# Kernel tuning notes

Measured on AMD Instinct MI355X. Metric: run time of the kernel, lower is better.

Reference implementation:

```python
import jax, jax.numpy as jnp
import numpy as np

N_HEADS = 16
HEAD_DIM = 64


def apply_rope(x, cos, sin):
    # x: [B, H, S, D]; cos/sin: [S, D//2]
    x_even = x[..., ::2]
    x_odd = x[..., 1::2]
    c = cos[None, None, :, :]
    s = sin[None, None, :, :]
    rot_even = x_even * c - x_odd * s
    rot_odd = x_even * s + x_odd * c
    return jnp.stack((rot_even, rot_odd), axis=-1).reshape(x.shape)


def setup_inputs() -> dict:
    key = jax.random.key(0)
    ks = jax.random.split(key, 7)
    B, S, D = 2, 2048, 1024
    x = jax.random.normal(ks[0], (B, S, D), dtype=jnp.float32)
    # realistic rope tables
    inv_freq = 1.0 / (10000.0 ** (np.arange(0, HEAD_DIM, 2, dtype=np.float32) / HEAD_DIM))
    t = np.arange(S, dtype=np.float32)
    freqs = np.outer(t, inv_freq)  # [S, HEAD_DIM//2]
    rope_cos = jnp.asarray(np.cos(freqs), dtype=jnp.float32)
    rope_sin = jnp.asarray(np.sin(freqs), dtype=jnp.float32)
    Wqkv = jax.random.normal(ks[1], (D, 3 * D), dtype=jnp.float32) * (D ** -0.5)
    bqkv = jax.random.normal(ks[2], (3 * D,), dtype=jnp.float32) * 0.02
    Wout = jax.random.normal(ks[3], (D, D), dtype=jnp.float32) * (D ** -0.5)
    bout = jax.random.normal(ks[4], (D,), dtype=jnp.float32) * 0.02
    return {"x": x, "rope_cos": rope_cos, "rope_sin": rope_sin,
            "Wqkv": Wqkv, "bqkv": bqkv, "Wout": Wout, "bout": bout}


def reference(x, rope_cos, rope_sin, Wqkv, bqkv, Wout, bout):
    B, S, D = x.shape
    H, Hd = N_HEADS, HEAD_DIM
    qkv = x @ Wqkv + bqkv                      # [B, S, 3D]
    qkv = qkv.reshape(B, S, 3, H, Hd).transpose(2, 0, 3, 1, 4)  # [3, B, H, S, Hd]
    q, k, v = qkv[0], qkv[1], qkv[2]
    q = apply_rope(q, rope_cos, rope_sin)
    k = apply_rope(k, rope_cos, rope_sin)
    scale = Hd ** -0.5
    scores = jnp.einsum('bhqd,bhkd->bhqk', q, k) * scale
    causal = jnp.tril(jnp.ones((S, S), dtype=bool))
    scores = jnp.where(causal[None, None], scores, jnp.finfo(scores.dtype).min)
    attn = jax.nn.softmax(scores, axis=-1)
    out = jnp.einsum('bhqk,bhkd->bhqd', attn, v)  # [B, H, S, Hd]
    out = out.transpose(0, 2, 1, 3).reshape(B, S, D)
    return out @ Wout + bout
```

## Files before the change

### kernel.cpp

```cpp
#include <hip/hip_runtime.h>
#include <hip/hip_bf16.h>

typedef unsigned short u16;
typedef __attribute__((ext_vector_type(4))) float f32x4;
typedef __attribute__((ext_vector_type(16))) float f32x16;
typedef __attribute__((ext_vector_type(8))) short short8;
typedef __attribute__((ext_vector_type(8))) unsigned short ushort8;

__device__ __forceinline__ u16 f2bf(float f) {
  union { float f; unsigned u; } v; v.f = f;
  unsigned r = v.u + 0x7fffu + ((v.u >> 16) & 1u);
  return (u16)(r >> 16);
}
__device__ __forceinline__ float b2f(u16 h) {
  union { unsigned u; float f; } v; v.u = ((unsigned)h) << 16;
  return v.f;
}
__device__ __forceinline__ f32x4 mfma16(short8 a, short8 b, f32x4 c) {
  return __builtin_amdgcn_mfma_f32_16x16x32_bf16(a, b, c, 0, 0, 0);
}
__device__ __forceinline__ f32x16 mfma32(short8 a, short8 b, f32x16 c) {
  return __builtin_amdgcn_mfma_f32_32x32x16_bf16(a, b, c, 0, 0, 0);
}
__device__ __forceinline__ unsigned cvtpk(float a, float b) {
  unsigned r;
  asm("v_cvt_pk_bf16_f32 %0, %1, %2" : "=v"(r) : "v"(a), "v"(b));
  return r;
}
__device__ __forceinline__ short8 pack4(unsigned w0, unsigned w1, unsigned w2, unsigned w3) {
  union { unsigned u[4]; short8 s; } t;
  t.u[0] = w0; t.u[1] = w1; t.u[2] = w2; t.u[3] = w3;
  return t.s;
}
__device__ __forceinline__ float exp2h(float x) { return __builtin_amdgcn_exp2f(x); }

__global__ __launch_bounds__(256) void cvt_f32_bf16_k(const float* __restrict__ in,
                                                      u16* __restrict__ out, int n8) {
  int t = blockIdx.x * 256 + threadIdx.x;
  if (t >= n8) return;
  const float4* p = (const float4*)(in + (size_t)t * 8);
  float4 a = p[0], b = p[1];
  ushort8 o;
  o[0] = f2bf(a.x); o[1] = f2bf(a.y); o[2] = f2bf(a.z); o[3] = f2bf(a.w);
  o[4] = f2bf(b.x); o[5] = f2bf(b.y); o[6] = f2bf(b.z); o[7] = f2bf(b.w);
  *(ushort8*)(out + (size_t)t * 8) = o;
}

__global__ __launch_bounds__(256) void transpose_f32_bf16_k(const float* __restrict__ in,
                                                            u16* __restrict__ out, int R, int C) {
  __shared__ float tile[32][33];
  int bc = blockIdx.x * 32, br = blockIdx.y * 32;
  int tx = threadIdx.x & 31, ty = threadIdx.x >> 5;
#pragma unroll
  for (int p = 0; p < 4; ++p)
    tile[ty + p * 8][tx] = in[(size_t)(br + ty + p * 8) * C + bc + tx];
  __syncthreads();
#pragma unroll
  for (int p = 0; p < 4; ++p)
    out[(size_t)(bc + ty + p * 8) * R + br + tx] = f2bf(tile[tx][ty + p * 8]);
}

template <int MODE>
__global__ __launch_bounds__(256) void gemm_bt_k(const u16* __restrict__ A,
                                                 const u16* __restrict__ Bt,
                                                 const float* __restrict__ bias,
                                                 const float* __restrict__ cosT,
                                                 const float* __restrict__ sinT,
                                                 void* __restrict__ Cout) {
  __shared__ __align__(16) u16 As[128 * 32];
  __shared__ __align__(16) u16 Bs[128 * 32];
  const int tid = threadIdx.x, lane = tid & 63, w = tid >> 6;
  const int wr = w >> 1, wc = w & 1, g = lane >> 4, c16 = lane & 15;
  const int rowBase = blockIdx.y * 128, colBase = blockIdx.x * 128;
  f32x4 acc[4][4] = {};
  const int e0 = (w * 2 + 0) * 512 + lane * 8;
  const int e1 = (w * 2 + 1) * 512 + lane * 8;
  const u16* Ag0 = A + (size_t)(rowBase + (e0 >> 5)) * 1024 + (e0 & 31);
  const u16* Ag1 = A + (size_t)(rowBase + (e1 >> 5)) * 1024 + (e1 & 31);
  const u16* Bg0 = Bt + (size_t)(colBase + (e0 >> 5)) * 1024 + (e0 & 31);
  const u16* Bg1 = Bt + (size_t)(colBase + (e1 >> 5)) * 1024 + (e1 & 31);
  u16* As0 = As + (w * 2 + 0) * 512;
  u16* As1 = As + (w * 2 + 1) * 512;
  u16* Bs0 = Bs + (w * 2 + 0) * 512;
  u16* Bs1 = Bs + (w * 2 + 1) * 512;
  for (int k0 = 0; k0 < 1024; k0 += 32) {
    __builtin_amdgcn_global_load_lds((const __attribute__((address_space(1))) void*)(Ag0 + k0),
                                     (__attribute__((address_space(3))) void*)As0, 16, 0, 0);
    __builtin_amdgcn_global_load_lds((const __attribute__((address_space(1))) void*)(Ag1 + k0),
                                     (__attribute__((address_space(3))) void*)As1, 16, 0, 0);
    __builtin_amdgcn_global_load_lds((const __attribute__((address_space(1))) void*)(Bg0 + k0),
                                     (__attribute__((address_space(3))) void*)Bs0, 16, 0, 0);
    __builtin_amdgcn_global_load_lds((const __attribute__((address_space(1))) void*)(Bg1 + k0),
                                     (__attribute__((address_space(3))) void*)Bs1, 16, 0, 0);
    asm volatile("s_waitcnt vmcnt(0)" ::: "memory");
    __syncthreads();
    short8 af[4], bfr[4];
#pragma unroll
    for (int t = 0; t < 4; ++t)
      af[t] = *(const short8*)(As + ((wr * 64 + t * 16 + c16) * 32 + g * 8));
#pragma unroll
    for (int t = 0; t < 4; ++t)
      bfr[t] = *(const short8*)(Bs + ((wc * 64 + t * 16 + c16) * 32 + g * 8));
#pragma unroll
    for (int i = 0; i < 4; ++i)
#pragma unroll
      for (int j = 0; j < 4; ++j) acc[i][j] = mfma16(af[i], bfr[j], acc[i][j]);
    __syncthreads();
  }
#pragma unroll
  for (int i = 0; i < 4; ++i) {
    int mbase = rowBase + wr * 64 + i * 16 + 4 * g;
#pragma unroll
    for (int j = 0; j < 4; ++j) {
      int n = colBase + wc * 64 + j * 16 + c16;
      float bv = bias[n];
#pragma unroll
      for (int r = 0; r < 4; ++r) {
        float v = acc[i][j][r] + bv;
        int m = mbase + r;
        if (MODE == 0) {
          int which = n >> 10, hh = (n >> 6) & 15, d = n & 63;
          int bb = m >> 11, s = m & 2047;
          float outv = v;
          if (which < 2) {
            float pv = __shfl_xor(v, 1);
            float cc = cosT[(size_t)s * 32 + (d >> 1)];
            float ss = sinT[(size_t)s * 32 + (d >> 1)];
            outv = (d & 1) ? (v * cc + pv * ss) : (v * cc - pv * ss);
            if (which == 0) outv *= 0.18033688f;
          }
          ((u16*)Cout)[((size_t)(((which * 2 + bb) * 16 + hh) * 2048 + s) << 6) + d] = f2bf(outv);
        } else {
          ((float*)Cout)[(size_t)m * 1024 + n] = v;
        }
      }
    }
  }
}

__global__ __launch_bounds__(256) void vtrans_k(const u16* __restrict__ V, u16* __restrict__ Vt) {
  __shared__ u16 t[64][72];
  const int bh = blockIdx.y, s0 = blockIdx.x * 64;
  const u16* src = V + ((size_t)bh << 17);
  u16* dst = Vt + ((size_t)bh << 17);
  const int r = threadIdx.x >> 2, c0 = (threadIdx.x & 3) * 16;
  *(short8*)&t[r][c0] = *(const short8*)(src + (size_t)(s0 + r) * 64 + c0);
  *(short8*)&t[r][c0 + 8] = *(const short8*)(src + (size_t)(s0 + r) * 64 + c0 + 8);
  __syncthreads();
  const int d = threadIdx.x >> 2, sc0 = (threadIdx.x & 3) * 16;
  ushort8 o0, o1;
#pragma unroll
  for (int e = 0; e < 8; ++e) { o0[e] = t[sc0 + e][d]; o1[e] = t[sc0 + 8 + e][d]; }
  *(ushort8*)(dst + (size_t)d * 2048 + s0 + sc0) = o0;
  *(ushort8*)(dst + (size_t)d * 2048 + s0 + sc0 + 8) = o1;
}

__global__ __launch_bounds__(512, 4) void attn6_k(const u16* __restrict__ Qm,
                                                  const u16* __restrict__ Km,
                                                  const u16* __restrict__ Vtm,
                                                  u16* __restrict__ Om) {
  __shared__ __align__(16) u16 smem[32768];
  u16* KL = smem;
  u16* VL = smem + 16384;

  const int tid = threadIdx.x;
  const int lane = tid & 63, w = tid >> 6;
  const int usub = w & 3, half = w >> 2;
  const int x = blockIdx.x & 7;
  const int idx = blockIdx.x >> 3;
  const int bh = 4 * x + (idx & 3);
  const int qmb = 15 - (idx >> 2);
  const int b = bh >> 4, hd = bh & 15;
  const int qb = qmb * 128 + usub * 32;
  const int q32 = lane & 31, hl = lane >> 5;
  const int NTH = qmb + 1;
  const int tbase = half * NTH;

  const u16* Qp = Qm + ((size_t)bh << 17);
  const u16* Kp = Km + ((size_t)bh << 17);
  const u16* Vtp = Vtm + ((size_t)bh << 17);

  const u16* qrow = Qp + ((size_t)(qb + q32) << 6) + 8 * hl;
  short8 qf[4];
#pragma unroll
  for (int ks = 0; ks < 4; ++ks) qf[ks] = *(const short8*)(qrow + 16 * ks);

  f32x16 acc0 = {}, acc1 = {};
  float m_run = -1e30f, l_run = 0.f;
  const int qg = qb + q32;
  const int r8 = lane >> 3, blk = lane & 7;
  const int swz = q32 & 7;

  auto stage = [&](int buf, int k0s) {
#pragma unroll
    for (int t = 0; t < 2; ++t) {
      const int c = usub * 2 + t;
      const int row = c * 8 + r8;
      const int sblk = blk ^ r8;
      const u16* ksrc = Kp + ((size_t)(k0s + row) << 6) + sblk * 8;
      __builtin_amdgcn_global_load_lds(
          (const __attribute__((address_space(1))) void*)ksrc,
          (__attribute__((address_space(3))) void*)(KL + (half * 2 + buf) * 4096 + c * 512),
          16, 0, 0);
      const u16* vsrc = Vtp + ((size_t)row << 11) + k0s + sblk * 8;
      __builtin_amdgcn_global_load_lds(
          (const __attribute__((address_space(1))) void*)vsrc,
          (__attribute__((address_space(3))) void*)(VL + (half * 2 + buf) * 4096 + c * 512),
          16, 0, 0);
    }
  };

  stage(0, 64 * tbase);
  asm volatile("s_waitcnt vmcnt(0)" ::: "memory");
  __syncthreads();

  for (int i = 0; i < NTH; ++i) {
    const int cur = i & 1;
    if (i + 1 < NTH) stage(cur ^ 1, 64 * (tbase + i + 1));
    const int k0 = 64 * (tbase + i);

    if (k0 <= qb + 31) {
      const u16* Kb = KL + (half * 2 + cur) * 4096;
      const u16* Vb = VL + (half * 2 + cur) * 4096;

      f32x16 s0 = {}, s1 = {};
      __builtin_amdgcn_s_setprio(1);
#pragma unroll
      for (int ks = 0; ks < 4; ++ks) {
        const int cb = ((2 * ks + hl) ^ swz) * 8;
        short8 kf0 = *(const short8*)(Kb + q32 * 64 + cb);
        short8 kf1 = *(const short8*)(Kb + (32 + q32) * 64 + cb);
        s0 = mfma32(kf0, qf[ks], s0);
        s1 = mfma32(kf1, qf[ks], s1);
      }
      __builtin_amdgcn_s_setprio(0);

      short8 vfa[4], vfb[4];
#pragma unroll
      for (int ks = 0; ks < 4; ++ks) {
        const int cb = ((2 * ks + hl) ^ swz) * 8;
        vfa[ks] = *(const short8*)(Vb + q32 * 64 + cb);
        vfb[ks] = *(const short8*)(Vb + (32 + q32) * 64 + cb);
      }

      if (k0 + 63 > qb) {
#pragma unroll
        for (int r = 0; r < 16; ++r) {
          const int kvl = k0 + (r & 3) + 8 * (r >> 2) + 4 * hl;
          s0[r] = (kvl <= qg) ? s0[r] : -1e30f;
          s1[r] = (kvl + 32 <= qg) ? s1[r] : -1e30f;
        }
      }

      float pmax = s0[0];
#pragma unroll
      for (int r = 1; r < 16; ++r) pmax = fmaxf(pmax, s0[r]);
#pragma unroll
      for (int r = 0; r < 16; ++r) pmax = fmaxf(pmax, s1[r]);
      pmax = fmaxf(pmax, __shfl_xor(pmax, 32));

      if (!__all(pmax <= m_run + 11.5f)) {
        const float mn = fmaxf(m_run, pmax);
        const float alpha = exp2h(m_run - mn);
        l_run *= alpha;
        m_run = mn;
#pragma unroll
        for (int r = 0; r < 16; ++r) {
          const int row = (r & 3) + 8 * (r >> 2) + 4 * hl;
          const float ar = __shfl(alpha, row);
          acc0[r] *= ar; acc1[r] *= ar;
        }
      }

      float rs = 0.f;
#pragma unroll
      for (int r = 0; r < 16; ++r) { s0[r] = exp2h(s0[r] - m_run); rs += s0[r]; }
#pragma unroll
      for (int r = 0; r < 16; ++r) { s1[r] = exp2h(s1[r] - m_run); rs += s1[r]; }
      rs += __shfl_xor(rs, 32);
      l_run += rs;

      short8 pa[4];
#pragma unroll
      for (int t = 0; t < 2; ++t) {
        float p0, p1, p2, p3, p4, p5, p6, p7, p8, p9, pa_, pb_, pc_, pd_, pe_, pf_;
        if (t == 0) {
          p0 = s0[0];  p1 = s0[1];  p2 = s0[2];  p3 = s0[3];
          p4 = s0[4];  p5 = s0[5];  p6 = s0[6];  p7 = s0[7];
          p8 = s0[8];  p9 = s0[9];  pa_ = s0[10]; pb_ = s0[11];
          pc_ = s0[12]; pd_ = s0[13]; pe_ = s0[14]; pf_ = s0[15];
        } else {
          p0 = s1[0];  p1 = s1[1];  p2 = s1[2];  p3 = s1[3];
          p4 = s1[4];  p5 = s1[5];  p6 = s1[6];  p7 = s1[7];
          p8 = s1[8];  p9 = s1[9];  pa_ = s1[10]; pb_ = s1[11];
          pc_ = s1[12]; pd_ = s1[13]; pe_ = s1[14]; pf_ = s1[15];
        }
        const unsigned a0 = cvtpk(p0, p1), a1 = cvtpk(p2, p3);
        const unsigned a2 = cvtpk(p4, p5), a3 = cvtpk(p6, p7);
        const unsigned b0 = cvtpk(p8, p9), b1 = cvtpk(pa_, pb_);
        const unsigned b2 = cvtpk(pc_, pd_), b3 = cvtpk(pe_, pf_);
        const unsigned r0 = __shfl_xor(hl ? a0 : a2, 32);
        const unsigned r1 = __shfl_xor(hl ? a1 : a3, 32);
        pa[2 * t] = hl ? pack4(r0, r1, a2, a3) : pack4(a0, a1, r0, r1);
        const unsigned r2 = __shfl_xor(hl ? b0 : b2, 32);
        const unsigned r3 = __shfl_xor(hl ? b1 : b3, 32);
        pa[2 * t + 1] = hl ? pack4(r2, r3, b2, b3) : pack4(b0, b1, r2, r3);
      }

      __builtin_amdgcn_s_setprio(1);
#pragma unroll
      for (int ks = 0; ks < 4; ++ks) {
        acc0 = mfma32(pa[ks], vfa[ks], acc0);
        acc1 = mfma32(pa[ks], vfb[ks], acc1);
      }
      __builtin_amdgcn_s_setprio(0);
    }

    asm volatile("s_waitcnt vmcnt(0)" ::: "memory");
    __syncthreads();
  }

  float* mbuf = (float*)(void*)smem;
  float* mu = mbuf + usub * (34 * 64);
  if (half == 1) {
    mu[lane] = m_run;
    mu[64 + lane] = l_run;
#pragma unroll
    for (int r = 0; r < 16; ++r) {
      mu[(2 + r) * 64 + lane] = acc0[r];
      mu[(18 + r) * 64 + lane] = acc1[r];
    }
  }
  __syncthreads();
  if (half == 0) {
    const float m_o = mu[lane];
    const float l_o = mu[64 + lane];
    const float M = fmaxf(m_run, m_o);
    const float ss = exp2h(m_run - M);
    const float so = exp2h(m_o - M);
    const float l_c = l_run * ss + l_o * so;
#pragma unroll
    for (int r = 0; r < 16; ++r) {
      const int row = (r & 3) + 8 * (r >> 2) + 4 * hl;
      const float ssr = __shfl(ss, row);
      const float sor = __shfl(so, row);
      const float li = 1.0f / __shfl(l_c, row);
      const float o0 = (acc0[r] * ssr + mu[(2 + r) * 64 + lane] * sor) * li;
      const float o1 = (acc1[r] * ssr + mu[(18 + r) * 64 + lane] * sor) * li;
      const int q = qb + row;
      const size_t base = ((size_t)(b * 2048 + q) << 10) + hd * 64 + q32;
      Om[base] = f2bf(o0);
      Om[base + 32] = f2bf(o1);
    }
  }
}

extern "C" void kernel_launch(void* const* d_in, const int* in_sizes, int n_in,
                              void* d_out, int out_size, void* d_ws, size_t ws_size,
                              hipStream_t stream) {
  const float* x        = (const float*)d_in[0];
  const float* rope_cos = (const float*)d_in[1];
  const float* rope_sin = (const float*)d_in[2];
  const float* Wqkv     = (const float*)d_in[3];
  const float* bqkv     = (const float*)d_in[4];
  const float* Wout     = (const float*)d_in[5];
  const float* bout     = (const float*)d_in[6];
  float* out = (float*)d_out;
  char* ws = (char*)d_ws;

  u16* Xb      = (u16*)(ws);
  u16* WqkvT   = (u16*)(ws + 8388608);
  u16* WoutT   = (u16*)(ws + 14680064);
  u16* QKV     = (u16*)(ws + 16777216);
  u16* AttnOut = (u16*)(ws + 41943040);
  u16* Vt      = (u16*)(ws + 50331648);

  cvt_f32_bf16_k<<<dim3(2048), dim3(256), 0, stream>>>(x, Xb, 524288);
  transpose_f32_bf16_k<<<dim3(96, 32), dim3(256), 0, stream>>>(Wqkv, WqkvT, 1024, 3072);
  transpose_f32_bf16_k<<<dim3(32, 32), dim3(256), 0, stream>>>(Wout, WoutT, 1024, 1024);

  gemm_bt_k<0><<<dim3(24, 32), dim3(256), 0, stream>>>(Xb, WqkvT, bqkv, rope_cos, rope_sin,
                                                       (void*)QKV);

  u16* Qw = QKV;
  u16* Kw = QKV + (size_t)4194304;
  u16* Vw = QKV + (size_t)8388608;
  vtrans_k<<<dim3(32, 32), dim3(256), 0, stream>>>(Vw, Vt);
  attn6_k<<<dim3(512), dim3(512), 0, stream>>>(Qw, Kw, Vt, AttnOut);

  gemm_bt_k<1><<<dim3(8, 32), dim3(256), 0, stream>>>(AttnOut, WoutT, bout, nullptr, nullptr, out);
}
```

Before: 155.9 us.

## Drop split-KV halves in attention; use 4-wave blocks with balanced causal tile order

The attention kernel no longer splits each 128-row query block's KV range across two 4-wave halves that are merged through shared memory at the end. Each 256-thread block now walks the whole causal KV range itself. Block-to-query-tile assignment is interleaved (largest tiles first, then smallest) to balance work, and the final merge is reduced to a single normalization. This removes the cross-half merge, its extra barrier and LDS traffic, and halves per-block LDS, at the cost of longer serial KV loops per block and less parallelism per query block.

```diff
diff --git a/kernel.cpp b/kernel.cpp
--- a/kernel.cpp
+++ b/kernel.cpp
@@ -155,26 +155,24 @@
   *(ushort8*)(dst + (size_t)d * 2048 + s0 + sc0 + 8) = o1;
 }
 
-__global__ __launch_bounds__(512, 4) void attn6_k(const u16* __restrict__ Qm,
+__global__ __launch_bounds__(256, 2) void attn7_k(const u16* __restrict__ Qm,
                                                   const u16* __restrict__ Km,
                                                   const u16* __restrict__ Vtm,
                                                   u16* __restrict__ Om) {
-  __shared__ __align__(16) u16 smem[32768];
-  u16* KL = smem;
-  u16* VL = smem + 16384;
+  __shared__ __align__(16) u16 KL[2][4096];
+  __shared__ __align__(16) u16 VL[2][4096];
 
   const int tid = threadIdx.x;
   const int lane = tid & 63, w = tid >> 6;
-  const int usub = w & 3, half = w >> 2;
   const int x = blockIdx.x & 7;
-  const int idx = blockIdx.x >> 3;
-  const int bh = 4 * x + (idx & 3);
-  const int qmb = 15 - (idx >> 2);
+  const int i = blockIdx.x >> 3;
+  const int bh = 4 * x + (i & 3);
+  const int rank = i >> 2;
+  const int qm = (rank < 8) ? (15 - rank) : (rank - 8);
   const int b = bh >> 4, hd = bh & 15;
-  const int qb = qmb * 128 + usub * 32;
+  const int qb = qm * 128 + w * 32;
   const int q32 = lane & 31, hl = lane >> 5;
-  const int NTH = qmb + 1;
-  const int tbase = half * NTH;
+  const int nt = 2 * qm + 2;
 
   const u16* Qp = Qm + ((size_t)bh << 17);
   const u16* Kp = Km + ((size_t)bh << 17);
@@ -188,40 +186,39 @@
   f32x16 acc0 = {}, acc1 = {};
   float m_run = -1e30f, l_run = 0.f;
   const int qg = qb + q32;
-  const int r8 = lane >> 3, blk = lane & 7;
+  const int rr = w * 8 + (lane >> 3);
+  const int sb = (lane & 7) ^ (lane >> 3);
   const int swz = q32 & 7;
 
   auto stage = [&](int buf, int k0s) {
-#pragma unroll
-    for (int t = 0; t < 2; ++t) {
-      const int c = usub * 2 + t;
-      const int row = c * 8 + r8;
-      const int sblk = blk ^ r8;
-      const u16* ksrc = Kp + ((size_t)(k0s + row) << 6) + sblk * 8;
-      __builtin_amdgcn_global_load_lds(
-          (const __attribute__((address_space(1))) void*)ksrc,
-          (__attribute__((address_space(3))) void*)(KL + (half * 2 + buf) * 4096 + c * 512),
-          16, 0, 0);
-      const u16* vsrc = Vtp + ((size_t)row << 11) + k0s + sblk * 8;
-      __builtin_amdgcn_global_load_lds(
-          (const __attribute__((address_space(1))) void*)vsrc,
-          (__attribute__((address_space(3))) void*)(VL + (half * 2 + buf) * 4096 + c * 512),
-          16, 0, 0);
-    }
+    u16* kb = &KL[buf][w * 512];
+    u16* vb = &VL[buf][w * 512];
+    __builtin_amdgcn_global_load_lds(
+        (const __attribute__((address_space(1))) void*)(Kp + ((size_t)(k0s + rr) << 6) + sb * 8),
+        (__attribute__((address_space(3))) void*)kb, 16, 0, 0);
+    __builtin_amdgcn_global_load_lds(
+        (const __attribute__((address_space(1))) void*)(Kp + ((size_t)(k0s + rr + 32) << 6) + sb * 8),
+        (__attribute__((address_space(3))) void*)(kb + 2048), 16, 0, 0);
+    __builtin_amdgcn_global_load_lds(
+        (const __attribute__((address_space(1))) void*)(Vtp + ((size_t)rr << 11) + k0s + sb * 8),
+        (__attribute__((address_space(3))) void*)vb, 16, 0, 0);
+    __builtin_amdgcn_global_load_lds(
+        (const __attribute__((address_space(1))) void*)(Vtp + ((size_t)(rr + 32) << 11) + k0s + sb * 8),
+        (__attribute__((address_space(3))) void*)(vb + 2048), 16, 0, 0);
   };
 
-  stage(0, 64 * tbase);
+  stage(0, 0);
   asm volatile("s_waitcnt vmcnt(0)" ::: "memory");
   __syncthreads();
 
-  for (int i = 0; i < NTH; ++i) {
-    const int cur = i & 1;
-    if (i + 1 < NTH) stage(cur ^ 1, 64 * (tbase + i + 1));
-    const int k0 = 64 * (tbase + i);
+  for (int it = 0; it < nt; ++it) {
+    const int cur = it & 1;
+    if (it + 1 < nt) stage(cur ^ 1, 64 * (it + 1));
+    const int k0 = 64 * it;
 
     if (k0 <= qb + 31) {
-      const u16* Kb = KL + (half * 2 + cur) * 4096;
-      const u16* Vb = VL + (half * 2 + cur) * 4096;
+      const u16* Kb = &KL[cur][0];
+      const u16* Vb = &VL[cur][0];
 
       f32x16 s0 = {}, s1 = {};
       __builtin_amdgcn_s_setprio(1);
@@ -320,38 +317,14 @@
     __syncthreads();
   }
 
-  float* mbuf = (float*)(void*)smem;
-  float* mu = mbuf + usub * (34 * 64);
-  if (half == 1) {
-    mu[lane] = m_run;
-    mu[64 + lane] = l_run;
-#pragma unroll
-    for (int r = 0; r < 16; ++r) {
-      mu[(2 + r) * 64 + lane] = acc0[r];
-      mu[(18 + r) * 64 + lane] = acc1[r];
-    }
-  }
-  __syncthreads();
-  if (half == 0) {
-    const float m_o = mu[lane];
-    const float l_o = mu[64 + lane];
-    const float M = fmaxf(m_run, m_o);
-    const float ss = exp2h(m_run - M);
-    const float so = exp2h(m_o - M);
-    const float l_c = l_run * ss + l_o * so;
-#pragma unroll
-    for (int r = 0; r < 16; ++r) {
-      const int row = (r & 3) + 8 * (r >> 2) + 4 * hl;
-      const float ssr = __shfl(ss, row);
-      const float sor = __shfl(so, row);
-      const float li = 1.0f / __shfl(l_c, row);
-      const float o0 = (acc0[r] * ssr + mu[(2 + r) * 64 + lane] * sor) * li;
-      const float o1 = (acc1[r] * ssr + mu[(18 + r) * 64 + lane] * sor) * li;
-      const int q = qb + row;
-      const size_t base = ((size_t)(b * 2048 + q) << 10) + hd * 64 + q32;
-      Om[base] = f2bf(o0);
-      Om[base + 32] = f2bf(o1);
-    }
+#pragma unroll
+  for (int r = 0; r < 16; ++r) {
+    const int row = (r & 3) + 8 * (r >> 2) + 4 * hl;
+    const float li = 1.0f / __shfl(l_run, row);
+    const int q = qb + row;
+    const size_t base = ((size_t)(b * 2048 + q) << 10) + hd * 64 + q32;
+    Om[base] = f2bf(acc0[r] * li);
+    Om[base + 32] = f2bf(acc1[r] * li);
   }
 }
 
@@ -386,7 +359,7 @@
   u16* Kw = QKV + (size_t)4194304;
   u16* Vw = QKV + (size_t)8388608;
   vtrans_k<<<dim3(32, 32), dim3(256), 0, stream>>>(Vw, Vt);
-  attn6_k<<<dim3(512), dim3(512), 0, stream>>>(Qw, Kw, Vt, AttnOut);
+  attn7_k<<<dim3(512), dim3(256), 0, stream>>>(Qw, Kw, Vt, AttnOut);
 
   gemm_bt_k<1><<<dim3(8, 32), dim3(256), 0, stream>>>(AttnOut, WoutT, bout, nullptr, nullptr, out);
 }
```

Result: faster. 138.2 us (-11.3%).
